# Performance work log

Hardware: AMD Instinct MI355X
Metric: run time of the kernel (lower is better)

## Reference

```python
import jax, jax.numpy as jnp
import numpy as np

GRID = 33
STRIDE = 2
HIDDEN = 256
N_LAYERS = 4
BATCH = 64
N_NODES = GRID * GRID  # 1089


def _stride_edges(g, s):
    """Replicates StrideGraphSAGE.stride_edge (including the strict j > s test)."""
    idx = np.arange(g * g).reshape(g, g)
    srcs, dsts = [], []
    # right neighbor: j < g - s
    srcs.append(idx[:, : g - s].ravel()); dsts.append(idx[:, s:].ravel())
    # down neighbor: i < g - s
    srcs.append(idx[: g - s, :].ravel()); dsts.append(idx[s:, :].ravel())
    # down-right: j < g - s and i < g - s
    srcs.append(idx[: g - s, : g - s].ravel()); dsts.append(idx[s:, s:].ravel())
    # down-left: j > s and i < g - s  (strict >, as in the original)
    srcs.append(idx[: g - s, s + 1 :].ravel()); dsts.append(idx[s:, 1 : g - s].ravel())
    return (np.concatenate(srcs).astype(np.int32),
            np.concatenate(dsts).astype(np.int32))


def setup_inputs() -> dict:
    key = jax.random.key(0)
    kx, kwl, kbl, kwr = jax.random.split(key, 4)
    x = jax.random.normal(kx, (BATCH, HIDDEN, GRID, GRID), dtype=jnp.float32)
    Wl = jax.random.normal(kwl, (N_LAYERS, HIDDEN, HIDDEN), dtype=jnp.float32) * 0.05
    bl = jax.random.normal(kbl, (N_LAYERS, HIDDEN), dtype=jnp.float32) * 0.05
    Wr = jax.random.normal(kwr, (N_LAYERS, HIDDEN, HIDDEN), dtype=jnp.float32) * 0.05
    src_np, dst_np = _stride_edges(GRID, STRIDE)
    return {
        "x": x, "Wl": Wl, "bl": bl, "Wr": Wr,
        "src": jnp.asarray(src_np), "dst": jnp.asarray(dst_np),
    }


def reference(x, Wl, bl, Wr, src, dst):
    B, C, H, W = x.shape
    N = H * W
    total = B * N
    # feature2graph: each image -> [N, C] node matrix, then batched -> [B*N, C]
    nodes = x.reshape(B, C, N).transpose(0, 2, 1).reshape(total, C)

    # The original passes the UNOFFSET single-graph edge_index to every layer,
    # so messages only flow among the first N rows; the rest get zero aggregate.
    deg = jnp.zeros((total,), x.dtype).at[dst].add(1.0)
    inv_deg = jnp.where(deg > 0, 1.0 / jnp.maximum(deg, 1.0), 0.0)[:, None]

    L = Wl.shape[0]
    outs = []
    for l in range(L):
        # SAGEConv (mean aggr): lin_l(mean_j x_src_j) + lin_r(x) ; every layer
        # is applied to the ORIGINAL node features (x is never updated).
        agg = jnp.zeros_like(nodes).at[dst].add(nodes[src]) * inv_deg
        h = agg @ Wl[l] + bl[l] + nodes @ Wr[l]
        h = jax.nn.elu(h)
        # graph2feature: raw contiguous view [N, C] -> (C, H, W) per graph
        outs.append(h.reshape(B, C, H, W))
    outs.append(x)
    return jnp.concatenate(outs, axis=1)
```

## Files before the change

### kernel.cpp

```cpp
#include <hip/hip_runtime.h>
#include <hip/hip_bf16.h>
#include <stdint.h>


#define C_DIM 256
#define GRID_G 33
#define N_NODES 1089
#define BATCH 64
#define TOTAL (BATCH * N_NODES)
#define M_PAD 69760
#define CN (C_DIM * N_NODES)
#define OUT_STRIDE_B (5 * CN)
#define NCOLS 1024
#define AGG_ROWS 1152

using bf16 = __hip_bfloat16;
typedef __attribute__((ext_vector_type(8))) short short8;
typedef __attribute__((ext_vector_type(4))) float f32x4;

#define NODES_BYTES ((size_t)M_PAD * C_DIM * 2)
#define OFF_NODES   ((size_t)0)
#define OFF_AGGB    (NODES_BYTES)
#define AGGB_BYTES  ((size_t)AGG_ROWS * C_DIM * 2)
#define OFF_WLT     (OFF_AGGB + AGGB_BYTES)
#define WT_BYTES    ((size_t)NCOLS * C_DIM * 2)
#define OFF_WRT     (OFF_WLT + WT_BYTES)

__device__ __forceinline__ void gload16(void* lds, const void* g) {
    __builtin_amdgcn_global_load_lds(
        (const __attribute__((address_space(1))) uint32_t*)g,
        (__attribute__((address_space(3))) uint32_t*)lds,
        16, 0, 0);
}

__global__ __launch_bounds__(256)
void prep_kernel(const float* __restrict__ x,
                 const float* __restrict__ Wl, const float* __restrict__ Wr,
                 bf16* __restrict__ nodes, bf16* __restrict__ WlT, bf16* __restrict__ WrT,
                 float* __restrict__ out)
{
    __shared__ char smem[33792];
    const int t = threadIdx.x;
    const int bid = blockIdx.x;
    if (bid < 128) {
        float (*tile)[65] = (float(*)[65])smem;
        const int sel = bid & 1;
        const int l = (bid >> 1) & 3;
        const int kt = ((bid >> 3) & 3) * 64;
        const int ct = ((bid >> 5) & 3) * 64;
        const float* W = sel ? Wr : Wl;
        bf16* WT = sel ? WrT : WlT;
        const int tc = t & 63;
        const int tk = t >> 6;
#pragma unroll
        for (int i = 0; i < 16; ++i) {
            int kl = i * 4 + tk;
            tile[kl][tc] = W[((size_t)(l * 256 + kt + kl)) * 256 + ct + tc];
        }
        __syncthreads();
#pragma unroll
        for (int i = 0; i < 16; ++i) {
            int cl = i * 4 + tk;
            WT[((size_t)(l * 256 + ct + cl)) * 256 + kt + tc] = __float2bfloat16(tile[tc][cl]);
        }
    } else {
        bf16 (*tile)[66] = (bf16(*)[66])smem;
        const int bid2 = bid - 128;
        const int b = bid2 / 18;
        const int n0 = (bid2 % 18) * 64;
        const int nl = t & 63;
        const int cs = t >> 6;
        const int n = n0 + nl;
        const bool nvalid = n < N_NODES;
        const float* xb = x + (size_t)b * CN;
        float* outb = out + (size_t)b * OUT_STRIDE_B + (size_t)4 * CN;
#pragma unroll 4
        for (int cc = 0; cc < 64; ++cc) {
            int c = cc * 4 + cs;
            if (nvalid) {
                float v = xb[(size_t)c * N_NODES + n];
                outb[(size_t)c * N_NODES + n] = v;
                tile[c][nl] = __float2bfloat16(v);
            }
        }
        __syncthreads();
        const int half = t >> 7;
        const int c0 = (t & 127) * 2;
#pragma unroll
        for (int it = 0; it < 32; ++it) {
            int row = it * 2 + half;
            int nr = n0 + row;
            if (nr < N_NODES) {
                __hip_bfloat162 p;
                p.x = tile[c0][row];
                p.y = tile[c0 + 1][row];
                *(__hip_bfloat162*)(nodes + ((size_t)b * N_NODES + nr) * C_DIM + c0) = p;
            }
        }
    }
}

__global__ __launch_bounds__(256)
void gather_kernel(const bf16* __restrict__ nodes, bf16* __restrict__ aggb)
{
    const int n = blockIdx.x;
    const int c = threadIdx.x;
    if (n >= N_NODES) {
        aggb[(size_t)n * C_DIM + c] = __float2bfloat16(0.f);
        return;
    }
    const int i = n / GRID_G, j = n % GRID_G;
    float s = 0.f, d = 0.f;
    if (j >= 2)           { s += __bfloat162float(nodes[(size_t)(n - 2)  * C_DIM + c]); d += 1.f; }
    if (i >= 2)           { s += __bfloat162float(nodes[(size_t)(n - 66) * C_DIM + c]); d += 1.f; }
    if (i >= 2 && j >= 2) { s += __bfloat162float(nodes[(size_t)(n - 68) * C_DIM + c]); d += 1.f; }
    if (i >= 2 && j >= 1 && j <= 30)
                          { s += __bfloat162float(nodes[(size_t)(n - 64) * C_DIM + c]); d += 1.f; }
    aggb[(size_t)n * C_DIM + c] = __float2bfloat16(d > 0.f ? s / d : 0.f);
}

__global__ __launch_bounds__(256, 4)
void gemm_kernel(const bf16* __restrict__ nodes, const bf16* __restrict__ agg,
                 const bf16* __restrict__ WrT, const bf16* __restrict__ WlT,
                 const float* __restrict__ bias, float* __restrict__ out)
{
    __shared__ bf16 Alds[2][128 * 32];
    __shared__ bf16 Blds[2][128 * 32];
    const int t = threadIdx.x;
    const int lane = t & 63;
    const int w = t >> 6;
    const unsigned bid = blockIdx.x;
    const unsigned swz = (bid & 7) * 545 + (bid >> 3);
    const int bcol = swz & 7;
    const int brow = swz >> 3;

    f32x4 acc[4][4] = {};

    const int tq = t >> 2;
    const int kk = (((t & 3) ^ ((tq >> 1) & 3)) << 3);
    const int wr = (w >> 1) << 6;
    const int wc = (w & 1) << 6;
    const int fr = lane & 15;
    const int kq = lane >> 4;
    const int swzr = (kq ^ ((fr >> 1) & 3)) << 3;

    char* AldsB = (char*)Alds;
    char* BldsB = (char*)Blds;
    const short* AldsS = (const short*)Alds;
    const short* BldsS = (const short*)Blds;

    const int nsteps = (brow * 128 < N_NODES) ? 16 : 8;
    const bf16* Abase0 = nodes + (size_t)brow * 128 * C_DIM;
    const bf16* Abase1 = agg + (size_t)brow * 128 * C_DIM;
    const bf16* Bbase0 = WrT + (size_t)bcol * 128 * C_DIM;
    const bf16* Bbase1 = WlT + (size_t)bcol * 128 * C_DIM;

    auto STAGE = [&](int s, int buf) {
        const int k0 = (s & 7) * 32;
        const bf16* Ag = (s < 8 ? Abase0 : Abase1) + (size_t)tq * C_DIM + k0 + kk;
        const bf16* Bg = (s < 8 ? Bbase0 : Bbase1) + (size_t)tq * C_DIM + k0 + kk;
        gload16(AldsB + buf * 8192 + w * 1024,        Ag);
        gload16(AldsB + buf * 8192 + 4096 + w * 1024, Ag + 64 * C_DIM);
        gload16(BldsB + buf * 8192 + w * 1024,        Bg);
        gload16(BldsB + buf * 8192 + 4096 + w * 1024, Bg + 64 * C_DIM);
    };

    STAGE(0, 0);
    for (int s = 0; s < nsteps; ++s) {
        asm volatile("s_waitcnt vmcnt(0)" ::: "memory");
        __builtin_amdgcn_s_barrier();
        if (s + 1 < nsteps) STAGE(s + 1, (s + 1) & 1);
        const short* Ab = AldsS + (s & 1) * 4096;
        const short* Bb = BldsS + (s & 1) * 4096;
        short8 av[4];
#pragma unroll
        for (int m = 0; m < 4; ++m)
            av[m] = *(const short8*)(Ab + (wr + m * 16 + fr) * 32 + swzr);
#pragma unroll
        for (int n = 0; n < 4; ++n) {
            short8 bv = *(const short8*)(Bb + (wc + n * 16 + fr) * 32 + swzr);
#pragma unroll
            for (int m = 0; m < 4; ++m)
                acc[m][n] = __builtin_amdgcn_mfma_f32_16x16x32_bf16(
                    av[m], bv, acc[m][n], 0, 0, 0);
        }
    }

    const int rq = kq * 4;
    const int r0 = brow * 128 + wr + rq;
    const unsigned bb0 = (unsigned)r0 / N_NODES;
    const int rsw = (int)((bb0 + 1) * N_NODES);
    const int colbase = bcol * 128 + wc + fr;
    size_t coff[4];
    float bi[4];
#pragma unroll
    for (int n = 0; n < 4; ++n) {
        int col = colbase + n * 16;
        coff[n] = (size_t)(col >> 8) * CN + (col & 255);
        bi[n] = bias[col];
    }
#pragma unroll
    for (int m = 0; m < 4; ++m) {
#pragma unroll
        for (int reg = 0; reg < 4; ++reg) {
            int r = r0 + m * 16 + reg;
            if (r < TOTAL) {
                int bb = (int)bb0 + (r >= rsw ? 1 : 0);
                int nn = r - bb * N_NODES;
                size_t base = (size_t)bb * OUT_STRIDE_B + (size_t)nn * C_DIM;
#pragma unroll
                for (int n = 0; n < 4; ++n) {
                    float v = acc[m][n][reg] + bi[n];
                    v = v > 0.f ? v : (__expf(v) - 1.0f);
                    out[base + coff[n]] = v;
                }
            }
        }
    }
}

extern "C" void kernel_launch(void* const* d_in, const int* in_sizes, int n_in,
                              void* d_out, int out_size, void* d_ws, size_t ws_size,
                              hipStream_t stream) {
    const float* x  = (const float*)d_in[0];
    const float* Wl = (const float*)d_in[1];
    const float* bl = (const float*)d_in[2];
    const float* Wr = (const float*)d_in[3];
    float* out = (float*)d_out;
    char* ws = (char*)d_ws;

    bf16* nodes = (bf16*)(ws + OFF_NODES);
    bf16* aggb  = (bf16*)(ws + OFF_AGGB);
    bf16* WlT   = (bf16*)(ws + OFF_WLT);
    bf16* WrT   = (bf16*)(ws + OFF_WRT);

    prep_kernel<<<128 + BATCH * 18, 256, 0, stream>>>(x, Wl, Wr, nodes, WlT, WrT, out);
    gather_kernel<<<AGG_ROWS, 256, 0, stream>>>(nodes, aggb);
    gemm_kernel<<<8 * 545, 256, 0, stream>>>(nodes, aggb, WrT, WlT, bl, out);
}
```

Before: 164.7 us.

## Enlarge GEMM tiles to 256x256 with 8-wave blocks and ping-pong LDS pipeline

Replaces the 128x128 tile, 4-wave GEMM with a 256x256 tile, 512-thread kernel that uses 128 KB of dynamic LDS holding double-buffered 64-wide K slices. Each K step is split into four quadrant phases that interleave half-tile prefetches with MFMA bursts under s_setprio and barriers. XCD-aware block swizzling is kept, and the aggregate buffer is padded to 1280 rows to cover the larger M tiles. The intent is more operand reuse per LDS load and less global traffic per FLOP, at the cost of fewer, larger workgroups, lower occupancy and more barriers.

New measurement: 159.8 us. 1.03x faster.

```diff
diff --git a/kernel.cpp b/kernel.cpp
--- a/kernel.cpp
+++ b/kernel.cpp
@@ -12,7 +12,9 @@
 #define CN (C_DIM * N_NODES)
 #define OUT_STRIDE_B (5 * CN)
 #define NCOLS 1024
-#define AGG_ROWS 1152
+#define AGG_ROWS_PAD 1280
+#define MT 273
+#define NWG (MT * 4)
 
 using bf16 = __hip_bfloat16;
 typedef __attribute__((ext_vector_type(8))) short short8;
@@ -21,7 +23,7 @@
 #define NODES_BYTES ((size_t)M_PAD * C_DIM * 2)
 #define OFF_NODES   ((size_t)0)
 #define OFF_AGGB    (NODES_BYTES)
-#define AGGB_BYTES  ((size_t)AGG_ROWS * C_DIM * 2)
+#define AGGB_BYTES  ((size_t)AGG_ROWS_PAD * C_DIM * 2)
 #define OFF_WLT     (OFF_AGGB + AGGB_BYTES)
 #define WT_BYTES    ((size_t)NCOLS * C_DIM * 2)
 #define OFF_WRT     (OFF_WLT + WT_BYTES)
@@ -119,100 +121,179 @@
     aggb[(size_t)n * C_DIM + c] = __float2bfloat16(d > 0.f ? s / d : 0.f);
 }
 
-__global__ __launch_bounds__(256, 4)
+__global__ __launch_bounds__(512)
 void gemm_kernel(const bf16* __restrict__ nodes, const bf16* __restrict__ agg,
                  const bf16* __restrict__ WrT, const bf16* __restrict__ WlT,
                  const float* __restrict__ bias, float* __restrict__ out)
 {
-    __shared__ bf16 Alds[2][128 * 32];
-    __shared__ bf16 Blds[2][128 * 32];
+    extern __shared__ char Sb[];
     const int t = threadIdx.x;
     const int lane = t & 63;
     const int w = t >> 6;
-    const unsigned bid = blockIdx.x;
-    const unsigned swz = (bid & 7) * 545 + (bid >> 3);
-    const int bcol = swz & 7;
-    const int brow = swz >> 3;
-
-    f32x4 acc[4][4] = {};
-
-    const int tq = t >> 2;
-    const int kk = (((t & 3) ^ ((tq >> 1) & 3)) << 3);
-    const int wr = (w >> 1) << 6;
-    const int wc = (w & 1) << 6;
+    const int wm = w >> 2;
+    const int wn = w & 3;
     const int fr = lane & 15;
     const int kq = lane >> 4;
-    const int swzr = (kq ^ ((fr >> 1) & 3)) << 3;
-
-    char* AldsB = (char*)Alds;
-    char* BldsB = (char*)Blds;
-    const short* AldsS = (const short*)Alds;
-    const short* BldsS = (const short*)Blds;
-
-    const int nsteps = (brow * 128 < N_NODES) ? 16 : 8;
-    const bf16* Abase0 = nodes + (size_t)brow * 128 * C_DIM;
-    const bf16* Abase1 = agg + (size_t)brow * 128 * C_DIM;
-    const bf16* Bbase0 = WrT + (size_t)bcol * 128 * C_DIM;
-    const bf16* Bbase1 = WlT + (size_t)bcol * 128 * C_DIM;
-
-    auto STAGE = [&](int s, int buf) {
-        const int k0 = (s & 7) * 32;
-        const bf16* Ag = (s < 8 ? Abase0 : Abase1) + (size_t)tq * C_DIM + k0 + kk;
-        const bf16* Bg = (s < 8 ? Bbase0 : Bbase1) + (size_t)tq * C_DIM + k0 + kk;
-        gload16(AldsB + buf * 8192 + w * 1024,        Ag);
-        gload16(AldsB + buf * 8192 + 4096 + w * 1024, Ag + 64 * C_DIM);
-        gload16(BldsB + buf * 8192 + w * 1024,        Bg);
-        gload16(BldsB + buf * 8192 + 4096 + w * 1024, Bg + 64 * C_DIM);
+
+    const unsigned bid = blockIdx.x;
+    const unsigned xcd = bid & 7, loc = bid >> 3;
+    const unsigned swz = (xcd < 4 ? xcd * 137u : 4u * 137u + (xcd - 4u) * 136u) + loc;
+    const int bcol = swz & 3;
+    const int brow = swz >> 2;
+
+    const int NT = (brow * 256 < N_NODES) ? 8 : 4;
+    const size_t Arow0 = (size_t)brow * 256;
+    const size_t Brow0 = (size_t)bcol * 256;
+
+    f32x4 acc[8][4] = {};
+
+    const int srow = t >> 3;
+    const int sk = (((t & 7) ^ (srow & 7)) << 3);
+    const int so0 = ((0 * 4 + kq) ^ (fr & 7)) << 4;
+    const int so1 = ((1 * 4 + kq) ^ (fr & 7)) << 4;
+    const int arow_b = (wm * 128 + fr) * 128;
+    const int brow_b = (wn * 64 + fr) * 128;
+
+    auto STAGE_HALF = [&](int kt, int half, int isB) {
+        const int buf = kt & 1;
+        const int kk0 = ((kt & 3) << 6) + sk;
+        if (!isB) {
+            const bf16* src = (kt < 4 ? nodes : agg);
+            const size_t gr = Arow0 + half * 128 + srow;
+            char* dst = Sb + buf * 32768 + half * 16384 + w * 1024;
+            gload16(dst,        src + gr * 256 + kk0);
+            gload16(dst + 8192, src + (gr + 64) * 256 + kk0);
+        } else {
+            const bf16* src = (kt < 4 ? WrT : WlT);
+            const size_t gr = Brow0 + half * 128 + srow;
+            char* dst = Sb + 65536 + buf * 32768 + half * 16384 + w * 1024;
+            gload16(dst,        src + gr * 256 + kk0);
+            gload16(dst + 8192, src + (gr + 64) * 256 + kk0);
+        }
     };
 
-    STAGE(0, 0);
-    for (int s = 0; s < nsteps; ++s) {
-        asm volatile("s_waitcnt vmcnt(0)" ::: "memory");
-        __builtin_amdgcn_s_barrier();
-        if (s + 1 < nsteps) STAGE(s + 1, (s + 1) & 1);
-        const short* Ab = AldsS + (s & 1) * 4096;
-        const short* Bb = BldsS + (s & 1) * 4096;
-        short8 av[4];
-#pragma unroll
-        for (int m = 0; m < 4; ++m)
-            av[m] = *(const short8*)(Ab + (wr + m * 16 + fr) * 32 + swzr);
-#pragma unroll
-        for (int n = 0; n < 4; ++n) {
-            short8 bv = *(const short8*)(Bb + (wc + n * 16 + fr) * 32 + swzr);
-#pragma unroll
-            for (int m = 0; m < 4; ++m)
-                acc[m][n] = __builtin_amdgcn_mfma_f32_16x16x32_bf16(
-                    av[m], bv, acc[m][n], 0, 0, 0);
-        }
-    }
-
-    const int rq = kq * 4;
-    const int r0 = brow * 128 + wr + rq;
+    STAGE_HALF(0, 0, 0); STAGE_HALF(0, 1, 0); STAGE_HALF(0, 0, 1); STAGE_HALF(0, 1, 1);
+    STAGE_HALF(1, 0, 0); STAGE_HALF(1, 1, 0); STAGE_HALF(1, 0, 1); STAGE_HALF(1, 1, 1);
+    asm volatile("s_waitcnt vmcnt(8)" ::: "memory");
+    __builtin_amdgcn_s_barrier();
+
+    short8 av[4][2], bv0[2][2], bv1[2][2];
+
+    for (int kt = 0; kt < NT; ++kt) {
+        const int ab = (kt & 1) * 32768;
+        const int bb = 65536 + (kt & 1) * 32768;
+        const bool pf = (kt + 1 < NT);
+
+#pragma unroll
+        for (int i = 0; i < 4; ++i) {
+            av[i][0] = *(const short8*)(Sb + ab + arow_b + i * 2048 + so0);
+            av[i][1] = *(const short8*)(Sb + ab + arow_b + i * 2048 + so1);
+        }
+#pragma unroll
+        for (int j = 0; j < 2; ++j) {
+            bv0[j][0] = *(const short8*)(Sb + bb + brow_b + j * 2048 + so0);
+            bv0[j][1] = *(const short8*)(Sb + bb + brow_b + j * 2048 + so1);
+        }
+        if (pf) STAGE_HALF(kt + 1, 0, 0);
+        __builtin_amdgcn_s_barrier();
+        asm volatile("s_waitcnt lgkmcnt(0)" ::: "memory");
+        __builtin_amdgcn_sched_barrier(0);
+        __builtin_amdgcn_s_setprio(1);
+#pragma unroll
+        for (int ks = 0; ks < 2; ++ks)
+#pragma unroll
+            for (int i = 0; i < 4; ++i)
+#pragma unroll
+                for (int j = 0; j < 2; ++j)
+                    acc[i][j] = __builtin_amdgcn_mfma_f32_16x16x32_bf16(
+                        av[i][ks], bv0[j][ks], acc[i][j], 0, 0, 0);
+        __builtin_amdgcn_s_setprio(0);
+        __builtin_amdgcn_s_barrier();
+
+#pragma unroll
+        for (int j = 0; j < 2; ++j) {
+            bv1[j][0] = *(const short8*)(Sb + bb + brow_b + 4096 + j * 2048 + so0);
+            bv1[j][1] = *(const short8*)(Sb + bb + brow_b + 4096 + j * 2048 + so1);
+        }
+        if (pf) STAGE_HALF(kt + 1, 1, 0);
+        __builtin_amdgcn_s_barrier();
+        asm volatile("s_waitcnt lgkmcnt(0)" ::: "memory");
+        __builtin_amdgcn_sched_barrier(0);
+        __builtin_amdgcn_s_setprio(1);
+#pragma unroll
+        for (int ks = 0; ks < 2; ++ks)
+#pragma unroll
+            for (int i = 0; i < 4; ++i)
+#pragma unroll
+                for (int j = 0; j < 2; ++j)
+                    acc[i][2 + j] = __builtin_amdgcn_mfma_f32_16x16x32_bf16(
+                        av[i][ks], bv1[j][ks], acc[i][2 + j], 0, 0, 0);
+        __builtin_amdgcn_s_setprio(0);
+        __builtin_amdgcn_s_barrier();
+
+#pragma unroll
+        for (int i = 0; i < 4; ++i) {
+            av[i][0] = *(const short8*)(Sb + ab + arow_b + 8192 + i * 2048 + so0);
+            av[i][1] = *(const short8*)(Sb + ab + arow_b + 8192 + i * 2048 + so1);
+        }
+        if (pf) STAGE_HALF(kt + 1, 0, 1);
+        __builtin_amdgcn_s_barrier();
+        asm volatile("s_waitcnt lgkmcnt(0)" ::: "memory");
+        __builtin_amdgcn_sched_barrier(0);
+        __builtin_amdgcn_s_setprio(1);
+#pragma unroll
+        for (int ks = 0; ks < 2; ++ks)
+#pragma unroll
+            for (int i = 0; i < 4; ++i)
+#pragma unroll
+                for (int j = 0; j < 2; ++j)
+                    acc[4 + i][2 + j] = __builtin_amdgcn_mfma_f32_16x16x32_bf16(
+                        av[i][ks], bv1[j][ks], acc[4 + i][2 + j], 0, 0, 0);
+        __builtin_amdgcn_s_setprio(0);
+        __builtin_amdgcn_s_barrier();
+
+        if (pf) STAGE_HALF(kt + 1, 1, 1);
+        __builtin_amdgcn_s_barrier();
+        __builtin_amdgcn_s_setprio(1);
+#pragma unroll
+        for (int ks = 0; ks < 2; ++ks)
+#pragma unroll
+            for (int i = 0; i < 4; ++i)
+#pragma unroll
+                for (int j = 0; j < 2; ++j)
+                    acc[4 + i][j] = __builtin_amdgcn_mfma_f32_16x16x32_bf16(
+                        av[i][ks], bv0[j][ks], acc[4 + i][j], 0, 0, 0);
+        __builtin_amdgcn_s_setprio(0);
+        if (pf) asm volatile("s_waitcnt vmcnt(0)" ::: "memory");
+        __builtin_amdgcn_s_barrier();
+    }
+
+    const int r0 = brow * 256 + wm * 128 + kq * 4;
     const unsigned bb0 = (unsigned)r0 / N_NODES;
     const int rsw = (int)((bb0 + 1) * N_NODES);
-    const int colbase = bcol * 128 + wc + fr;
-    size_t coff[4];
+    float* outL = out + (size_t)bcol * CN;
+    int cof[4];
     float bi[4];
 #pragma unroll
-    for (int n = 0; n < 4; ++n) {
-        int col = colbase + n * 16;
-        coff[n] = (size_t)(col >> 8) * CN + (col & 255);
-        bi[n] = bias[col];
-    }
-#pragma unroll
-    for (int m = 0; m < 4; ++m) {
+    for (int nf = 0; nf < 4; ++nf) {
+        int c = wn * 64 + nf * 16 + fr;
+        cof[nf] = c;
+        bi[nf] = bias[bcol * 256 + c];
+    }
+#pragma unroll
+    for (int mf = 0; mf < 8; ++mf) {
 #pragma unroll
         for (int reg = 0; reg < 4; ++reg) {
-            int r = r0 + m * 16 + reg;
+            int r = r0 + mf * 16 + reg;
             if (r < TOTAL) {
                 int bb = (int)bb0 + (r >= rsw ? 1 : 0);
                 int nn = r - bb * N_NODES;
                 size_t base = (size_t)bb * OUT_STRIDE_B + (size_t)nn * C_DIM;
 #pragma unroll
-                for (int n = 0; n < 4; ++n) {
-                    float v = acc[m][n][reg] + bi[n];
+                for (int nf = 0; nf < 4; ++nf) {
+                    float v = acc[mf][nf][reg] + bi[nf];
                     v = v > 0.f ? v : (__expf(v) - 1.0f);
-                    out[base + coff[n]] = v;
+                    outL[base + cof[nf]] = v;
                 }
             }
         }
@@ -235,6 +316,6 @@
     bf16* WrT   = (bf16*)(ws + OFF_WRT);
 
     prep_kernel<<<128 + BATCH * 18, 256, 0, stream>>>(x, Wl, Wr, nodes, WlT, WrT, out);
-    gather_kernel<<<AGG_ROWS, 256, 0, stream>>>(nodes, aggb);
-    gemm_kernel<<<8 * 545, 256, 0, stream>>>(nodes, aggb, WrT, WlT, bl, out);
-}
+    gather_kernel<<<AGG_ROWS_PAD, 256, 0, stream>>>(nodes, aggb);
+    gemm_kernel<<<NWG, 512, 131072, stream>>>(nodes, aggb, WrT, WlT, bl, out);
+}
```

## Make GEMM persistent per column strip with Wr held in registers

Applied to the files above, without the earlier changes.

The GEMM becomes a persistent grid of 512 blocks. Each block owns one 128-column strip and walks about 8-9 row tiles. The whole Wr fragment for its strip is loaded once into registers (8x4 short8 per lane), so only A tiles stream through a 3-stage LDS ring. The aggregated rows use Wl fragments read directly from global memory. This removes the repeated B-tile loads and per-tile launch overhead, at the cost of high register pressure (launch bounds lowered to 2 waves), possible spills, and a smaller grid.

New measurement: 225.9 us. 1.37x slower.

```diff
diff --git a/kernel.cpp b/kernel.cpp
--- a/kernel.cpp
+++ b/kernel.cpp
@@ -119,102 +119,145 @@
     aggb[(size_t)n * C_DIM + c] = __float2bfloat16(d > 0.f ? s / d : 0.f);
 }
 
-__global__ __launch_bounds__(256, 4)
+__global__ __launch_bounds__(256, 2)
 void gemm_kernel(const bf16* __restrict__ nodes, const bf16* __restrict__ agg,
                  const bf16* __restrict__ WrT, const bf16* __restrict__ WlT,
                  const float* __restrict__ bias, float* __restrict__ out)
 {
-    __shared__ bf16 Alds[2][128 * 32];
-    __shared__ bf16 Blds[2][128 * 32];
+    __shared__ bf16 Ar[3][128 * 32];
     const int t = threadIdx.x;
     const int lane = t & 63;
     const int w = t >> 6;
-    const unsigned bid = blockIdx.x;
-    const unsigned swz = (bid & 7) * 545 + (bid >> 3);
-    const int bcol = swz & 7;
-    const int brow = swz >> 3;
-
-    f32x4 acc[4][4] = {};
-
-    const int tq = t >> 2;
-    const int kk = (((t & 3) ^ ((tq >> 1) & 3)) << 3);
+    const int bs = (int)(blockIdx.x & 63);
+    const int strip = (int)(blockIdx.x >> 6);
+
     const int wr = (w >> 1) << 6;
     const int wc = (w & 1) << 6;
     const int fr = lane & 15;
     const int kq = lane >> 4;
     const int swzr = (kq ^ ((fr >> 1) & 3)) << 3;
-
-    char* AldsB = (char*)Alds;
-    char* BldsB = (char*)Blds;
-    const short* AldsS = (const short*)Alds;
-    const short* BldsS = (const short*)Blds;
-
-    const int nsteps = (brow * 128 < N_NODES) ? 16 : 8;
-    const bf16* Abase0 = nodes + (size_t)brow * 128 * C_DIM;
-    const bf16* Abase1 = agg + (size_t)brow * 128 * C_DIM;
-    const bf16* Bbase0 = WrT + (size_t)bcol * 128 * C_DIM;
-    const bf16* Bbase1 = WlT + (size_t)bcol * 128 * C_DIM;
-
-    auto STAGE = [&](int s, int buf) {
-        const int k0 = (s & 7) * 32;
-        const bf16* Ag = (s < 8 ? Abase0 : Abase1) + (size_t)tq * C_DIM + k0 + kk;
-        const bf16* Bg = (s < 8 ? Bbase0 : Bbase1) + (size_t)tq * C_DIM + k0 + kk;
-        gload16(AldsB + buf * 8192 + w * 1024,        Ag);
-        gload16(AldsB + buf * 8192 + 4096 + w * 1024, Ag + 64 * C_DIM);
-        gload16(BldsB + buf * 8192 + w * 1024,        Bg);
-        gload16(BldsB + buf * 8192 + 4096 + w * 1024, Bg + 64 * C_DIM);
+    const int tq = t >> 2;
+    const int kk = (((t & 3) ^ ((tq >> 1) & 3)) << 3);
+    const size_t stoff = (size_t)tq * C_DIM + kk;
+
+    char* ArB = (char*)Ar;
+    const short* ArS = (const short*)Ar;
+
+    const bf16* Bp = WrT + ((size_t)(strip * 128 + wc + fr)) * C_DIM + kq * 8;
+    short8 bv[8][4];
+#pragma unroll
+    for (int ks = 0; ks < 8; ++ks)
+#pragma unroll
+        for (int nf = 0; nf < 4; ++nf)
+            bv[ks][nf] = *(const short8*)(Bp + (size_t)nf * 16 * C_DIM + ks * 32);
+    const bf16* Lp = WlT + ((size_t)(strip * 128 + wc + fr)) * C_DIM + kq * 8;
+
+    const int nbrow = (bs < 33) ? 9 : 8;
+    const bool hasMix = (bs < 9);
+    const int nj = nbrow + (hasMix ? 1 : 0);
+
+    f32x4 acc[4][4] = {};
+
+    auto decode = [&](int j, int& brw, bool& isAgg) {
+        if (hasMix) { isAgg = (j == 1); brw = (j <= 1) ? bs : bs + 64 * (j - 1); }
+        else        { isAgg = false;    brw = bs + 64 * j; }
     };
 
-    STAGE(0, 0);
-    for (int s = 0; s < nsteps; ++s) {
-        asm volatile("s_waitcnt vmcnt(0)" ::: "memory");
-        __builtin_amdgcn_s_barrier();
-        if (s + 1 < nsteps) STAGE(s + 1, (s + 1) & 1);
-        const short* Ab = AldsS + (s & 1) * 4096;
-        const short* Bb = BldsS + (s & 1) * 4096;
-        short8 av[4];
-#pragma unroll
-        for (int m = 0; m < 4; ++m)
-            av[m] = *(const short8*)(Ab + (wr + m * 16 + fr) * 32 + swzr);
-#pragma unroll
-        for (int n = 0; n < 4; ++n) {
-            short8 bv = *(const short8*)(Bb + (wc + n * 16 + fr) * 32 + swzr);
+    {
+        int brw0; bool a0; decode(0, brw0, a0);
+        const bf16* A0 = nodes + (size_t)brw0 * 128 * C_DIM + stoff;
+        gload16(ArB + 0 * 8192 + w * 1024,        A0);
+        gload16(ArB + 0 * 8192 + 4096 + w * 1024, A0 + 64 * C_DIM);
+        gload16(ArB + 1 * 8192 + w * 1024,        A0 + 32);
+        gload16(ArB + 1 * 8192 + 4096 + w * 1024, A0 + 64 * C_DIM + 32);
+    }
+    asm volatile("s_waitcnt vmcnt(0)" ::: "memory");
+    __builtin_amdgcn_s_barrier();
+
+    int rb = 0;
+    for (int j = 0; j < nj; ++j) {
+        int brw; bool isAgg; decode(j, brw, isAgg);
+        const bool doEpi = !(hasMix && j == 0);
+        const bf16* Ac = (isAgg ? agg : nodes) + (size_t)brw * 128 * C_DIM + stoff;
+        int brwN; bool aggN;
+        if (j + 1 < nj) decode(j + 1, brwN, aggN); else { brwN = brw; aggN = isAgg; }
+        const bf16* An = (aggN ? agg : nodes) + (size_t)brwN * 128 * C_DIM + stoff;
+
+#pragma unroll
+        for (int ss = 0; ss < 8; ++ss) {
+            asm volatile("s_waitcnt vmcnt(2)" ::: "memory");
+            __builtin_amdgcn_s_barrier();
+            const int wb = (rb == 0) ? 2 : ((rb == 1) ? 0 : 1);
+            if (ss < 6) {
+                gload16(ArB + wb * 8192 + w * 1024,        Ac + (ss + 2) * 32);
+                gload16(ArB + wb * 8192 + 4096 + w * 1024, Ac + 64 * C_DIM + (ss + 2) * 32);
+            } else {
+                gload16(ArB + wb * 8192 + w * 1024,        An + (ss - 6) * 32);
+                gload16(ArB + wb * 8192 + 4096 + w * 1024, An + 64 * C_DIM + (ss - 6) * 32);
+            }
+            short8 av[4];
 #pragma unroll
             for (int m = 0; m < 4; ++m)
-                acc[m][n] = __builtin_amdgcn_mfma_f32_16x16x32_bf16(
-                    av[m], bv, acc[m][n], 0, 0, 0);
-        }
-    }
-
-    const int rq = kq * 4;
-    const int r0 = brow * 128 + wr + rq;
-    const unsigned bb0 = (unsigned)r0 / N_NODES;
-    const int rsw = (int)((bb0 + 1) * N_NODES);
-    const int colbase = bcol * 128 + wc + fr;
-    size_t coff[4];
-    float bi[4];
-#pragma unroll
-    for (int n = 0; n < 4; ++n) {
-        int col = colbase + n * 16;
-        coff[n] = (size_t)(col >> 8) * CN + (col & 255);
-        bi[n] = bias[col];
-    }
-#pragma unroll
-    for (int m = 0; m < 4; ++m) {
-#pragma unroll
-        for (int reg = 0; reg < 4; ++reg) {
-            int r = r0 + m * 16 + reg;
-            if (r < TOTAL) {
-                int bb = (int)bb0 + (r >= rsw ? 1 : 0);
-                int nn = r - bb * N_NODES;
-                size_t base = (size_t)bb * OUT_STRIDE_B + (size_t)nn * C_DIM;
-#pragma unroll
-                for (int n = 0; n < 4; ++n) {
-                    float v = acc[m][n][reg] + bi[n];
-                    v = v > 0.f ? v : (__expf(v) - 1.0f);
-                    out[base + coff[n]] = v;
+                av[m] = *(const short8*)(ArS + rb * 4096 + (wr + m * 16 + fr) * 32 + swzr);
+            if (isAgg) {
+                short8 bl[4];
+#pragma unroll
+                for (int nf = 0; nf < 4; ++nf)
+                    bl[nf] = *(const short8*)(Lp + (size_t)nf * 16 * C_DIM + ss * 32);
+#pragma unroll
+                for (int m = 0; m < 4; ++m)
+#pragma unroll
+                    for (int n = 0; n < 4; ++n)
+                        acc[m][n] = __builtin_amdgcn_mfma_f32_16x16x32_bf16(
+                            av[m], bl[n], acc[m][n], 0, 0, 0);
+            } else {
+#pragma unroll
+                for (int m = 0; m < 4; ++m)
+#pragma unroll
+                    for (int n = 0; n < 4; ++n)
+                        acc[m][n] = __builtin_amdgcn_mfma_f32_16x16x32_bf16(
+                            av[m], bv[ss][n], acc[m][n], 0, 0, 0);
+            }
+            rb = (rb == 2) ? 0 : rb + 1;
+        }
+
+        if (doEpi) {
+            const int rq = kq * 4;
+            const int r0 = brw * 128 + wr + rq;
+            const unsigned bb0 = (unsigned)r0 / N_NODES;
+            const int rsw = (int)((bb0 + 1) * N_NODES);
+            const int colbase = strip * 128 + wc + fr;
+            size_t coff[4];
+            float bi[4];
+#pragma unroll
+            for (int n = 0; n < 4; ++n) {
+                int col = colbase + n * 16;
+                coff[n] = (size_t)(col >> 8) * CN + (col & 255);
+                bi[n] = bias[col];
+            }
+#pragma unroll
+            for (int m = 0; m < 4; ++m) {
+#pragma unroll
+                for (int reg = 0; reg < 4; ++reg) {
+                    int r = r0 + m * 16 + reg;
+                    if (r < TOTAL) {
+                        int bb = (int)bb0 + (r >= rsw ? 1 : 0);
+                        int nn = r - bb * N_NODES;
+                        size_t base = (size_t)bb * OUT_STRIDE_B + (size_t)nn * C_DIM;
+#pragma unroll
+                        for (int n = 0; n < 4; ++n) {
+                            float v = acc[m][n][reg] + bi[n];
+                            v = v > 0.f ? v : (__expf(v) - 1.0f);
+                            out[base + coff[n]] = v;
+                        }
+                    }
                 }
             }
+#pragma unroll
+            for (int m = 0; m < 4; ++m)
+#pragma unroll
+                for (int n = 0; n < 4; ++n)
+                    acc[m][n] = (f32x4){0.f, 0.f, 0.f, 0.f};
         }
     }
 }
@@ -236,5 +279,5 @@
 
     prep_kernel<<<128 + BATCH * 18, 256, 0, stream>>>(x, Wl, Wr, nodes, WlT, WrT, out);
     gather_kernel<<<AGG_ROWS, 256, 0, stream>>>(nodes, aggb);
-    gemm_kernel<<<8 * 545, 256, 0, stream>>>(nodes, aggb, WrT, WlT, bl, out);
-}
+    gemm_kernel<<<512, 256, 0, stream>>>(nodes, aggb, WrT, WlT, bl, out);
+}
```
